# Kernel optimization log

Hardware: AMD Instinct MI355X
Metric: run time of the kernel (lower is better)

The kernel has to match this reference:

```python
import jax, jax.numpy as jnp
import numpy as np

NUM_TASKS = 5
POOL = 5
R = 8
TOPK = 3
SCALE = 1.0  # module self.scale and forward scale arg, both 1
B, S, DIN, DOUT = 4, 4096, 1024, 1024


def setup_inputs() -> dict:
    key = jax.random.key(0)
    ks = jax.random.split(key, 5)
    inp = {
        "input": jax.random.normal(ks[0], (B, S, DIN), dtype=jnp.float32),
        "W": jax.random.normal(ks[1], (DOUT, DIN), dtype=jnp.float32) / np.sqrt(DIN),
        "lora_down": jax.random.normal(ks[2], (POOL, DIN, R), dtype=jnp.float32) / np.sqrt(DIN),
        "lora_up": jax.random.normal(ks[3], (POOL, R, DOUT), dtype=jnp.float32) / np.sqrt(R),
        "lora_route": jax.random.normal(ks[4], (NUM_TASKS, DIN, POOL), dtype=jnp.float32) * 0.02,
        "task_id": 4,
    }
    return inp


def reference(input, W, lora_down, lora_up, lora_route, task_id):
    # Eval branch (self.training == False), 1 <= task_id <= num_tasks.
    task_id = min(task_id, NUM_TASKS)
    k = min(task_id, TOPK)
    route = lora_route[1]                          # [DIN, POOL] (detach split is a no-op for fwd)
    input_mean = jnp.mean(input, axis=1)           # [B, DIN]
    lora_omegas = jnp.mean(input_mean @ route, axis=0)  # [POOL]
    sliced = lora_omegas[1:task_id + 1]            # source slices from 1
    G, I = jax.lax.top_k(sliced, k)                # indices used DIRECTLY (as in source)
    gate = jax.nn.softmax(G)                       # [k]
    # detached expert products (eval path detaches lora_down @ lora_up)
    dw = jax.lax.stop_gradient(
        jnp.einsum('kdr,kro->kdo', lora_down[I], lora_up[I]))  # [k, DIN, DOUT]
    # delta = sum_i gate[i] * SCALE * (input @ dw[i]); forward scale arg = 1
    delta = SCALE * jnp.einsum('k,bsd,kdo->bso', gate, input, dw)
    # delta_w_all[:B//2] = 0
    bmask = (jnp.arange(input.shape[0]) >= input.shape[0] // 2).astype(delta.dtype)
    delta = delta * bmask[:, None, None]
    return input @ W.T + delta
```

## Files before the change

kernel.cpp:

```cpp
#include <hip/hip_runtime.h>
#include <hip/hip_bf16.h>

typedef __attribute__((ext_vector_type(8))) __bf16 bf16x8;
typedef __attribute__((ext_vector_type(4))) __bf16 bf16x4;
typedef __attribute__((ext_vector_type(4))) float f32x4;

#define DIN 1024
#define DOUT 1024
#define BB 4
#define SS 4096
#define MROWS (BB*SS)
#define POOLN 5
#define RR 8
#define NTASKS 5
#define TOPKK 3

__global__ __launch_bounds__(256) void k1a_stream(const float* __restrict__ in,
                                                  __bf16* __restrict__ inB,
                                                  float* __restrict__ partial) {
    const int t = threadIdx.x;
    const int b = blockIdx.x;
    const int idx0 = b * 256 + t;
    const float4* __restrict__ inv = (const float4*)in;
    bf16x4* __restrict__ outv = (bf16x4*)inB;

    float s0 = 0.f, s1 = 0.f, s2 = 0.f, s3 = 0.f;
    size_t idx = idx0;
    float4 cur = inv[idx];
#pragma unroll
    for (int it = 0; it < 8; ++it) {
        float4 nxt = cur;
        if (it < 7) nxt = inv[idx + 524288];
        s0 += cur.x; s1 += cur.y; s2 += cur.z; s3 += cur.w;
        bf16x4 bb = { (__bf16)cur.x, (__bf16)cur.y, (__bf16)cur.z, (__bf16)cur.w };
        outv[idx] = bb;
        cur = nxt;
        idx += 524288;
    }
    float4 p = { s0, s1, s2, s3 };
    *(float4*)&partial[(size_t)b * DIN + t * 4] = p;
}

__global__ __launch_bounds__(256) void k1b_reduce(const float* __restrict__ partial,
                                                  float* __restrict__ colsum) {
    const int tid = blockIdx.x * 256 + threadIdx.x;
    const int c = tid & (DIN - 1);
    const int g = tid >> 10;
    float s = 0.f;
    const int b0 = g * 256;
#pragma unroll 8
    for (int b = b0; b < b0 + 256; ++b)
        s += partial[(size_t)b * DIN + c];
    atomicAdd(&colsum[c], s);
}

__global__ void k2_gate(const float* __restrict__ colsum,
                        const float* __restrict__ lroute,
                        const int* __restrict__ task_id_p,
                        float* __restrict__ gate, int* __restrict__ gidx) {
    const int l = threadIdx.x;
    float part[POOLN] = {0.f, 0.f, 0.f, 0.f, 0.f};
    for (int d = l; d < DIN; d += 64) {
        const float cs = colsum[d] * (1.0f / (float)MROWS);
        const float* rp = &lroute[(size_t)1 * DIN * POOLN + (size_t)d * POOLN];
#pragma unroll
        for (int p = 0; p < POOLN; ++p) part[p] += cs * rp[p];
    }
#pragma unroll
    for (int p = 0; p < POOLN; ++p) {
        float v = part[p];
        for (int off = 32; off; off >>= 1) v += __shfl_down(v, off);
        part[p] = v;
    }
    if (l == 0) {
        int tid = *task_id_p;
        if (tid > NTASKS) tid = NTASKS;
        int L = tid < (POOLN - 1) ? tid : (POOLN - 1);
        int k = tid < TOPKK ? tid : TOPKK;
        float sl[POOLN];
        for (int j = 0; j < L; ++j) sl[j] = part[1 + j];
        float G[TOPKK]; int I[TOPKK];
        int used = 0;
        for (int j = 0; j < k; ++j) {
            int best = -1; float bv = 0.f;
            for (int i2 = 0; i2 < L; ++i2) {
                if (used & (1 << i2)) continue;
                if (best < 0 || sl[i2] > bv) { bv = sl[i2]; best = i2; }
            }
            used |= 1 << best; G[j] = bv; I[j] = best;
        }
        if (k > 0) {
            float m = G[0];
            float e[TOPKK]; float se = 0.f;
            for (int j = 0; j < k; ++j) { e[j] = expf(G[j] - m); se += e[j]; }
            for (int j = 0; j < k; ++j) { gate[j] = e[j] / se; gidx[j] = I[j]; }
        }
        for (int j = k; j < TOPKK; ++j) { gate[j] = 0.f; gidx[j] = 0; }
    }
}

__global__ __launch_bounds__(256) void k3_weights(const float* __restrict__ W,
                                                  const float* __restrict__ ldown,
                                                  const float* __restrict__ lup,
                                                  const float* __restrict__ gate,
                                                  const int* __restrict__ gidx,
                                                  __bf16* __restrict__ Wb0,
                                                  __bf16* __restrict__ Wb1) {
    const int o = blockIdx.x;
    const int t = threadIdx.x;
    float c[TOPKK][RR];
#pragma unroll
    for (int j = 0; j < TOPKK; ++j) {
        const float g = gate[j];
        const int   p = gidx[j];
#pragma unroll
        for (int r = 0; r < RR; ++r)
            c[j][r] = g * lup[(size_t)p * RR * DOUT + (size_t)r * DOUT + o];
    }
    const int d0 = t * 4;
    const float4 wv = *(const float4*)&W[(size_t)o * DIN + d0];
    float outv[4] = { wv.x, wv.y, wv.z, wv.w };
    float dwv[4]  = { 0.f, 0.f, 0.f, 0.f };
#pragma unroll
    for (int j = 0; j < TOPKK; ++j) {
        const int p = gidx[j];
#pragma unroll
        for (int dd = 0; dd < 4; ++dd) {
            const float4 da = *(const float4*)&ldown[(size_t)p * DIN * RR + (size_t)(d0 + dd) * RR];
            const float4 db = *(const float4*)&ldown[(size_t)p * DIN * RR + (size_t)(d0 + dd) * RR + 4];
            dwv[dd] += da.x * c[j][0] + da.y * c[j][1] + da.z * c[j][2] + da.w * c[j][3]
                     + db.x * c[j][4] + db.y * c[j][5] + db.z * c[j][6] + db.w * c[j][7];
        }
    }
    bf16x4 b0 = { (__bf16)outv[0], (__bf16)outv[1], (__bf16)outv[2], (__bf16)outv[3] };
    bf16x4 b1 = { (__bf16)(outv[0] + dwv[0]), (__bf16)(outv[1] + dwv[1]),
                  (__bf16)(outv[2] + dwv[2]), (__bf16)(outv[3] + dwv[3]) };
    *(bf16x4*)&Wb0[(size_t)o * DIN + d0] = b0;
    *(bf16x4*)&Wb1[(size_t)o * DIN + d0] = b1;
}

__global__ __launch_bounds__(256) void k4_gemm(const __bf16* __restrict__ A,
                                               const __bf16* __restrict__ B0,
                                               const __bf16* __restrict__ B1,
                                               float* __restrict__ C) {
    __shared__ ushort As[128 * 64];
    __shared__ ushort Bs[128 * 64];
    const int bid = blockIdx.x;
    const int tn  = (bid >> 3) & 7;
    const int tm  = (bid & 7) + 8 * (bid >> 6);
    const __hip_bfloat16* __restrict__ dummy = nullptr; (void)dummy;
    const __bf16* __restrict__ Bt = (tm >= 64) ? B1 : B0;
    const int lane = threadIdx.x & 63;
    const int wid  = threadIdx.x >> 6;
    const int wm = wid >> 1, wn = wid & 1;

    const int lr = lane >> 3;
    const int lk = (lane & 7) ^ lr;

    f32x4 acc[4][4];
#pragma unroll
    for (int i = 0; i < 4; ++i)
#pragma unroll
        for (int j = 0; j < 4; ++j) acc[i][j] = (f32x4){0.f, 0.f, 0.f, 0.f};

    const size_t abase = (size_t)tm * 128 * 1024;
    const size_t bbase = (size_t)tn * 128 * 1024;

    auto stage = [&](int kt) {
#pragma unroll
        for (int i = 0; i < 4; ++i) {
            const int c   = wid * 4 + i;
            const int row = c * 8 + lr;
            const __bf16* ga = A  + abase + (size_t)row * 1024 + (size_t)kt * 64 + lk * 8;
            const __bf16* gb = Bt + bbase + (size_t)row * 1024 + (size_t)kt * 64 + lk * 8;
            __builtin_amdgcn_global_load_lds((const __attribute__((address_space(1))) void*)ga,
                                             (__attribute__((address_space(3))) void*)&As[c * 512],
                                             16, 0, 0);
            __builtin_amdgcn_global_load_lds((const __attribute__((address_space(1))) void*)gb,
                                             (__attribute__((address_space(3))) void*)&Bs[c * 512],
                                             16, 0, 0);
        }
    };

    stage(0);
#pragma unroll 1
    for (int kt = 0; kt < 16; ++kt) {
        __syncthreads();
#pragma unroll
        for (int ks = 0; ks < 2; ++ks) {
            bf16x8 af[4], bfr[4];
            const int chb = (ks * 4 + (lane >> 4)) ^ (lane & 7);
#pragma unroll
            for (int mi = 0; mi < 4; ++mi) {
                const int row = wm * 64 + mi * 16 + (lane & 15);
                af[mi] = *(const bf16x8*)&As[row * 64 + chb * 8];
            }
#pragma unroll
            for (int ni = 0; ni < 4; ++ni) {
                const int row = wn * 64 + ni * 16 + (lane & 15);
                bfr[ni] = *(const bf16x8*)&Bs[row * 64 + chb * 8];
            }
#pragma unroll
            for (int mi = 0; mi < 4; ++mi)
#pragma unroll
                for (int ni = 0; ni < 4; ++ni)
                    acc[mi][ni] = __builtin_amdgcn_mfma_f32_16x16x32_bf16(
                        af[mi], bfr[ni], acc[mi][ni], 0, 0, 0);
        }
        __syncthreads();
        if (kt < 15) stage(kt + 1);
    }

#pragma unroll
    for (int mi = 0; mi < 4; ++mi) {
#pragma unroll
        for (int r = 0; r < 4; ++r) {
            const int grow = tm * 128 + wm * 64 + mi * 16 + (lane >> 4) * 4 + r;
            float* cp = C + (size_t)grow * 1024 + tn * 128 + wn * 64 + (lane & 15);
#pragma unroll
            for (int ni = 0; ni < 4; ++ni) cp[ni * 16] = acc[mi][ni][r];
        }
    }
}

extern "C" void kernel_launch(void* const* d_in, const int* in_sizes, int n_in,
                              void* d_out, int out_size, void* d_ws, size_t ws_size,
                              hipStream_t stream) {
    const float* in     = (const float*)d_in[0];
    const float* W      = (const float*)d_in[1];
    const float* ldown  = (const float*)d_in[2];
    const float* lup    = (const float*)d_in[3];
    const float* lroute = (const float*)d_in[4];
    const int*   taskid = (const int*)d_in[5];
    float* out = (float*)d_out;

    __bf16* inB   = (__bf16*)d_ws;
    __bf16* Wb0   = inB + (size_t)MROWS * DIN;
    __bf16* Wb1   = Wb0 + (size_t)DOUT * DIN;
    float*  colsum= (float*)(Wb1 + (size_t)DOUT * DIN);
    float*  gate  = colsum + DIN;
    int*    gidx  = (int*)(gate + TOPKK);

    float* partial = out;

    hipMemsetAsync(colsum, 0, DIN * sizeof(float), stream);
    k1a_stream<<<2048, 256, 0, stream>>>(in, inB, partial);
    k1b_reduce<<<32, 256, 0, stream>>>(partial, colsum);
    k2_gate<<<1, 64, 0, stream>>>(colsum, lroute, taskid, gate, gidx);
    k3_weights<<<1024, 256, 0, stream>>>(W, ldown, lup, gate, gidx, Wb0, Wb1);
    k4_gemm<<<1024, 256, 0, stream>>>(inB, Wb0, Wb1, out);
}
```

Before: 105.5 us.

## Rewrite bf16 GEMM with 256x256 tiles, 4-stage LDS pipeline and XCD-aware mapping

Moves the main GEMM to 256x256 output tiles computed by 512 threads (8 waves), so each block reuses its loaded A and B data more. It streams K in 32-wide slabs through a 4-deep LDS ring buffer filled by direct global-to-LDS loads, with explicit vmcnt waits, so memory latency overlaps with MFMA work. It also remaps block indices so neighbouring tiles land on the same XCD, and raises wave priority around the MFMA burst. The cost is about 128KB of LDS and many more accumulators per thread, which limits occupancy to one block per CU, and the hand-counted wait values and swizzle must be exactly right.

```diff
diff --git a/kernel.cpp b/kernel.cpp
--- a/kernel.cpp
+++ b/kernel.cpp
@@ -139,84 +139,104 @@
     *(bf16x4*)&Wb1[(size_t)o * DIN + d0] = b1;
 }
 
-__global__ __launch_bounds__(256) void k4_gemm(const __bf16* __restrict__ A,
+__global__ __launch_bounds__(512) void k4_gemm(const __bf16* __restrict__ A,
                                                const __bf16* __restrict__ B0,
                                                const __bf16* __restrict__ B1,
                                                float* __restrict__ C) {
-    __shared__ ushort As[128 * 64];
-    __shared__ ushort Bs[128 * 64];
+    __shared__ ushort lds[65536];
     const int bid = blockIdx.x;
-    const int tn  = (bid >> 3) & 7;
-    const int tm  = (bid & 7) + 8 * (bid >> 6);
-    const __hip_bfloat16* __restrict__ dummy = nullptr; (void)dummy;
-    const __bf16* __restrict__ Bt = (tm >= 64) ? B1 : B0;
+    const int xcd = bid & 7;
+    const int idx = bid >> 3;
+    const int tm  = xcd * 8 + (idx >> 2);
+    const int tn  = idx & 3;
+    const __bf16* __restrict__ Bt = (tm >= 32) ? B1 : B0;
+
     const int lane = threadIdx.x & 63;
     const int wid  = threadIdx.x >> 6;
-    const int wm = wid >> 1, wn = wid & 1;
-
-    const int lr = lane >> 3;
-    const int lk = (lane & 7) ^ lr;
-
-    f32x4 acc[4][4];
-#pragma unroll
-    for (int i = 0; i < 4; ++i)
+    const int wm = wid >> 2, wn = wid & 3;
+
+    const int rpl  = lane >> 3;
+    const int sl   = (lane & 7) ^ rpl;
+    const int srow = rpl * 2 + (sl >> 2);
+    const int sc   = sl & 3;
+
+    const char* gA = (const char*)A  + ((size_t)(tm*256 + wid*32 + srow)) * 2048 + sc * 16;
+    const char* gB = (const char*)Bt + ((size_t)(tn*256 + wid*32 + srow)) * 2048 + sc * 16;
+    const int ldsAst = wid * 1024;
+    const int ldsBst = 8192 + wid * 1024;
+
+    const int rhalf = (lane & 15) >> 1;
+    const int slot  = ((lane >> 4) + 4 * (lane & 1)) ^ rhalf;
+    const int aoff  = (wm * 64 + rhalf) * 64 + slot * 8;
+    const int boff  = 8192 + (wn * 32 + rhalf) * 64 + slot * 8;
+
+    f32x4 acc[8][4];
+#pragma unroll
+    for (int i = 0; i < 8; ++i)
 #pragma unroll
         for (int j = 0; j < 4; ++j) acc[i][j] = (f32x4){0.f, 0.f, 0.f, 0.f};
 
-    const size_t abase = (size_t)tm * 128 * 1024;
-    const size_t bbase = (size_t)tn * 128 * 1024;
-
-    auto stage = [&](int kt) {
-#pragma unroll
-        for (int i = 0; i < 4; ++i) {
-            const int c   = wid * 4 + i;
-            const int row = c * 8 + lr;
-            const __bf16* ga = A  + abase + (size_t)row * 1024 + (size_t)kt * 64 + lk * 8;
-            const __bf16* gb = Bt + bbase + (size_t)row * 1024 + (size_t)kt * 64 + lk * 8;
-            __builtin_amdgcn_global_load_lds((const __attribute__((address_space(1))) void*)ga,
-                                             (__attribute__((address_space(3))) void*)&As[c * 512],
-                                             16, 0, 0);
-            __builtin_amdgcn_global_load_lds((const __attribute__((address_space(1))) void*)gb,
-                                             (__attribute__((address_space(3))) void*)&Bs[c * 512],
-                                             16, 0, 0);
+    auto stageSlab = [&](int s) {
+        const int p = s & 3;
+        const size_t kb = (size_t)s * 64;
+#pragma unroll
+        for (int j = 0; j < 2; ++j) {
+            __builtin_amdgcn_global_load_lds(
+                (const __attribute__((address_space(1))) void*)(gA + (size_t)j * 32768 + kb),
+                (__attribute__((address_space(3))) void*)&lds[p * 16384 + ldsAst + j * 512],
+                16, 0, 0);
+            __builtin_amdgcn_global_load_lds(
+                (const __attribute__((address_space(1))) void*)(gB + (size_t)j * 32768 + kb),
+                (__attribute__((address_space(3))) void*)&lds[p * 16384 + ldsBst + j * 512],
+                16, 0, 0);
         }
     };
 
-    stage(0);
+    auto computeSlab = [&](int s) {
+        const int p = s & 3;
+        const ushort* aB = &lds[p * 16384 + aoff];
+        const ushort* bB = &lds[p * 16384 + boff];
+        bf16x8 a[8], b[4];
+#pragma unroll
+        for (int mi = 0; mi < 8; ++mi) a[mi] = *(const bf16x8*)(aB + mi * 512);
+#pragma unroll
+        for (int ni = 0; ni < 4; ++ni) b[ni] = *(const bf16x8*)(bB + ni * 512);
+        __builtin_amdgcn_s_setprio(1);
+#pragma unroll
+        for (int mi = 0; mi < 8; ++mi)
+#pragma unroll
+            for (int ni = 0; ni < 4; ++ni)
+                acc[mi][ni] = __builtin_amdgcn_mfma_f32_16x16x32_bf16(
+                    a[mi], b[ni], acc[mi][ni], 0, 0, 0);
+        __builtin_amdgcn_s_setprio(0);
+    };
+
+    stageSlab(0); stageSlab(1); stageSlab(2);
+
+#define K4_STEP(S, NSTR, DOSTAGE)                                     \
+    {                                                                 \
+        if (DOSTAGE) stageSlab((S) + 3);                              \
+        asm volatile("s_waitcnt vmcnt(" NSTR ")" ::: "memory");       \
+        __builtin_amdgcn_s_barrier();                                 \
+        asm volatile("" ::: "memory");                                \
+        computeSlab(S);                                               \
+        asm volatile("" ::: "memory");                                \
+        __builtin_amdgcn_s_barrier();                                 \
+    }
+
 #pragma unroll 1
-    for (int kt = 0; kt < 16; ++kt) {
-        __syncthreads();
-#pragma unroll
-        for (int ks = 0; ks < 2; ++ks) {
-            bf16x8 af[4], bfr[4];
-            const int chb = (ks * 4 + (lane >> 4)) ^ (lane & 7);
-#pragma unroll
-            for (int mi = 0; mi < 4; ++mi) {
-                const int row = wm * 64 + mi * 16 + (lane & 15);
-                af[mi] = *(const bf16x8*)&As[row * 64 + chb * 8];
-            }
-#pragma unroll
-            for (int ni = 0; ni < 4; ++ni) {
-                const int row = wn * 64 + ni * 16 + (lane & 15);
-                bfr[ni] = *(const bf16x8*)&Bs[row * 64 + chb * 8];
-            }
-#pragma unroll
-            for (int mi = 0; mi < 4; ++mi)
-#pragma unroll
-                for (int ni = 0; ni < 4; ++ni)
-                    acc[mi][ni] = __builtin_amdgcn_mfma_f32_16x16x32_bf16(
-                        af[mi], bfr[ni], acc[mi][ni], 0, 0, 0);
-        }
-        __syncthreads();
-        if (kt < 15) stage(kt + 1);
-    }
-
-#pragma unroll
-    for (int mi = 0; mi < 4; ++mi) {
+    for (int s = 0; s < 29; ++s) K4_STEP(s, "12", true);
+    K4_STEP(29, "8", false);
+    K4_STEP(30, "4", false);
+    K4_STEP(31, "0", false);
+#undef K4_STEP
+
+#pragma unroll
+    for (int mi = 0; mi < 8; ++mi) {
 #pragma unroll
         for (int r = 0; r < 4; ++r) {
-            const int grow = tm * 128 + wm * 64 + mi * 16 + (lane >> 4) * 4 + r;
-            float* cp = C + (size_t)grow * 1024 + tn * 128 + wn * 64 + (lane & 15);
+            const int grow = tm * 256 + wm * 128 + mi * 16 + (lane >> 4) * 4 + r;
+            float* cp = C + (size_t)grow * 1024 + tn * 256 + wn * 64 + (lane & 15);
 #pragma unroll
             for (int ni = 0; ni < 4; ++ni) cp[ni * 16] = acc[mi][ni][r];
         }
@@ -248,5 +268,5 @@
     k1b_reduce<<<32, 256, 0, stream>>>(partial, colsum);
     k2_gate<<<1, 64, 0, stream>>>(colsum, lroute, taskid, gate, gidx);
     k3_weights<<<1024, 256, 0, stream>>>(W, ldown, lup, gate, gidx, Wb0, Wb1);
-    k4_gemm<<<1024, 256, 0, stream>>>(inB, Wb0, Wb1, out);
-}
+    k4_gemm<<<256, 512, 0, stream>>>(inB, Wb0, Wb1, out);
+}
```

Result: faster. 102.4 us (-2.9%).
